# Optimization experiments

Measured on AMD Instinct MI355X. Metric: run time of the kernel, lower is better.

The kernel has to match this reference:

```python
import jax, jax.numpy as jnp
import numpy as np

N, D = 20000, 16          # nodes, fixed in-degree
IN, HID, OUT = 128, 128, 1


def _lstm_final_h(x_seq, Wih, Whh, bih, bhh):
    # x_seq: [D, N, F]; LSTM with hidden size H == F, zero init state.
    # Returns final hidden state h_D: [N, H]. PyTorch gate order i,f,g,o.
    Nn = x_seq.shape[1]
    H = Whh.shape[1]
    b = bih + bhh

    def step(carry, xt):
        h, c = carry
        gates = xt @ Wih.T + h @ Whh.T + b          # [N, 4H]
        i, f, g, o = jnp.split(gates, 4, axis=-1)
        c = jax.nn.sigmoid(f) * c + jax.nn.sigmoid(i) * jnp.tanh(g)
        h = jax.nn.sigmoid(o) * jnp.tanh(c)
        return (h, c), None

    init = (jnp.zeros((Nn, H), x_seq.dtype), jnp.zeros((Nn, H), x_seq.dtype))
    (h, _), _ = jax.lax.scan(step, init, x_seq)
    return h


def _sage_lstm(x, nbr_idx, Wih, Whh, bih, bhh, Wself, Wneigh, bneigh):
    # DGL SAGEConv(aggregator='lstm'): out = fc_self(x) + fc_neigh(lstm(neighbors))
    msgs = x[nbr_idx]                                # gather: [N, D, F]
    hN = _lstm_final_h(jnp.swapaxes(msgs, 0, 1), Wih, Whh, bih, bhh)  # [N, F]
    return x @ Wself.T + hN @ Wneigh.T + bneigh


def setup_inputs() -> dict:
    key = jax.random.key(0)
    ks = jax.random.split(key, 16)
    s = 1.0 / float(np.sqrt(IN))
    u = lambda k, sh: jax.random.uniform(k, sh, jnp.float32, -s, s)
    return {
        "x": jax.random.normal(ks[0], (N, IN), jnp.float32),
        "nbr_idx": jax.random.randint(ks[1], (N, D), 0, N),
        "Wih1": u(ks[2], (4 * IN, IN)), "Whh1": u(ks[3], (4 * IN, IN)),
        "bih1": u(ks[4], (4 * IN,)), "bhh1": u(ks[5], (4 * IN,)),
        "Wself1": u(ks[6], (HID, IN)), "Wneigh1": u(ks[7], (HID, IN)),
        "bneigh1": jnp.zeros((HID,), jnp.float32),
        "Wih2": u(ks[8], (4 * HID, HID)), "Whh2": u(ks[9], (4 * HID, HID)),
        "bih2": u(ks[10], (4 * HID,)), "bhh2": u(ks[11], (4 * HID,)),
        "Wself2": u(ks[12], (OUT, HID)), "Wneigh2": u(ks[13], (OUT, HID)),
        "bneigh2": jnp.zeros((OUT,), jnp.float32),
    }


def reference(x, nbr_idx, Wih1, Whh1, bih1, bhh1, Wself1, Wneigh1, bneigh1,
              Wih2, Whh2, bih2, bhh2, Wself2, Wneigh2, bneigh2):
    h = _sage_lstm(x, nbr_idx, Wih1, Whh1, bih1, bhh1, Wself1, Wneigh1, bneigh1)
    h = jax.nn.relu(h)
    h = _sage_lstm(h, nbr_idx, Wih2, Whh2, bih2, bhh2, Wself2, Wneigh2, bneigh2)
    return jax.nn.sigmoid(h)
```

## Files before the change

### kernel.cpp

```cpp
#include <hip/hip_runtime.h>


#define NN   20000
#define L2E  1.4426950408889634f

typedef unsigned short u16;
typedef __attribute__((ext_vector_type(8))) short frag8;
typedef __attribute__((ext_vector_type(4))) float facc4;
typedef __attribute__((ext_vector_type(8))) _Float16 half8;

#define OFF_X16   0u
#define OFF_H1    5120000u
#define OFF_WIH1P 15360000u
#define OFF_WHH1P 15491072u
#define OFF_WIH2P 15622144u
#define OFF_WHH2P 15753216u
#define OFF_WS1P  15884288u
#define OFF_WN1P  15917056u
#define OFF_WS2B  15949824u
#define OFF_WN2B  15950080u
#define OFF_B1    15950336u
#define OFF_B2    15952384u
#define OFF_XPREA 15954432u
#define OFF_XPREB 36434432u

__device__ __forceinline__ u16 f2bf(float f) {
  union { float f; unsigned u; } v; v.f = f;
  unsigned r = (v.u + 0x7fffu + ((v.u >> 16) & 1u)) >> 16;
  return (u16)r;
}
__device__ __forceinline__ float bflo(unsigned u) {
  union { unsigned u; float f; } v; v.u = u << 16; return v.f;
}
__device__ __forceinline__ float bfhi(unsigned u) {
  union { unsigned u; float f; } v; v.u = u & 0xffff0000u; return v.f;
}
__device__ __forceinline__ unsigned pk2h(float a, float b) {
  union { _Float16 h[2]; unsigned u; } v;
  v.h[0] = (_Float16)a; v.h[1] = (_Float16)b;
  return v.u;
}
__device__ __forceinline__ unsigned pkbf(float a, float b) {
  unsigned r;
  asm("v_cvt_pk_bf16_f32 %0, %1, %2" : "=v"(r) : "v"(a), "v"(b));
  return r;
}
__device__ __forceinline__ facc4 mfma16(frag8 a, frag8 b, facc4 c) {
  return __builtin_amdgcn_mfma_f32_16x16x32_bf16(a, b, c, 0, 0, 0);
}
__device__ __forceinline__ float rcpf(float x) { return __builtin_amdgcn_rcpf(x); }
__device__ __forceinline__ float ex2(float x)  { return __builtin_amdgcn_exp2f(x); }
__device__ __forceinline__ float sigm_ps(float xp) { return rcpf(1.f + ex2(-xp)); }
__device__ __forceinline__ float gate_scale(int row) {
  return (row >= 256 && row < 384) ? 2.f * L2E : L2E;
}
__device__ __forceinline__ float dot2(unsigned a, unsigned b) {
  return bflo(a) * bflo(b) + bfhi(a) * bfhi(b);
}

__device__ __forceinline__ void pack512v(frag8* dst, const float* src, int f) {
  int ln = f & 63, kb = (f >> 6) & 3, tj = f >> 8;
  int row = tj * 16 + (ln & 15);
  int col = kb * 32 + (ln >> 4) * 8;
  float s = gate_scale(row);
  const float* p = src + row * 128 + col;
  float4 v0 = *(const float4*)p;
  float4 v1 = *(const float4*)(p + 4);
  uint4 u = { pkbf(v0.x * s, v0.y * s), pkbf(v0.z * s, v0.w * s),
              pkbf(v1.x * s, v1.y * s), pkbf(v1.z * s, v1.w * s) };
  *(uint4*)&dst[f] = u;
}
__device__ __forceinline__ void pack128v(frag8* dst, const float* src, int f) {
  int ln = f & 63, kb = (f >> 6) & 3, tj = f >> 8;
  const float* p = src + (tj * 16 + (ln & 15)) * 128 + kb * 32 + (ln >> 4) * 8;
  float4 v0 = *(const float4*)p;
  float4 v1 = *(const float4*)(p + 4);
  uint4 u = { pkbf(v0.x, v0.y), pkbf(v0.z, v0.w),
              pkbf(v1.x, v1.y), pkbf(v1.z, v1.w) };
  *(uint4*)&dst[f] = u;
}

__global__ __launch_bounds__(256) void pack_kernel(
    const float* __restrict__ Wih1, const float* __restrict__ Whh1,
    const float* __restrict__ bih1, const float* __restrict__ bhh1,
    const float* __restrict__ Wself1, const float* __restrict__ Wneigh1,
    const float* __restrict__ Wih2, const float* __restrict__ Whh2,
    const float* __restrict__ bih2, const float* __restrict__ bhh2,
    const float* __restrict__ Wself2, const float* __restrict__ Wneigh2,
    char* __restrict__ ws)
{
  int i = blockIdx.x * 256 + threadIdx.x;
  if (i < 8192) { pack512v((frag8*)(ws + OFF_WIH1P), Wih1, i); return; }
  i -= 8192;
  if (i < 8192) { pack512v((frag8*)(ws + OFF_WHH1P), Whh1, i); return; }
  i -= 8192;
  if (i < 8192) { pack512v((frag8*)(ws + OFF_WIH2P), Wih2, i); return; }
  i -= 8192;
  if (i < 8192) { pack512v((frag8*)(ws + OFF_WHH2P), Whh2, i); return; }
  i -= 8192;
  if (i < 2048) { pack128v((frag8*)(ws + OFF_WS1P), Wself1, i); return; }
  i -= 2048;
  if (i < 2048) { pack128v((frag8*)(ws + OFF_WN1P), Wneigh1, i); return; }
  i -= 2048;
  if (i < 128) { ((u16*)(ws + OFF_WS2B))[i] = f2bf(Wself2[i]); return; }
  i -= 128;
  if (i < 128) { ((u16*)(ws + OFF_WN2B))[i] = f2bf(Wneigh2[i]); return; }
  i -= 128;
  if (i < 512) { ((float*)(ws + OFF_B1))[i] = (bih1[i] + bhh1[i]) * gate_scale(i); return; }
  i -= 512;
  if (i < 512) { ((float*)(ws + OFF_B2))[i] = (bih2[i] + bhh2[i]) * gate_scale(i); }
}

__global__ __launch_bounds__(512) void prep1_kernel(
    const float* __restrict__ x,
    const frag8* __restrict__ Wp,
    const float* __restrict__ bias,
    u16* __restrict__ x16,
    u16* __restrict__ xpre)
{
  __shared__ __align__(16) u16 xt[32 * 136];
  __shared__ __align__(16) u16 stage[32 * 520];
  const int tid = threadIdx.x;
  const int base = blockIdx.x * 32;
  {
    int r = tid >> 4, o = (tid & 15) * 8;
    const float* src = x + (size_t)(base + r) * 128 + o;
    float4 v0 = *(const float4*)(src);
    float4 v1 = *(const float4*)(src + 4);
    uint4 st = { pkbf(v0.x, v0.y), pkbf(v0.z, v0.w),
                 pkbf(v1.x, v1.y), pkbf(v1.z, v1.w) };
    *(uint4*)(xt + r * 136 + o) = st;
    *(uint4*)(x16 + (size_t)(base + r) * 128 + o) = st;
  }
  __syncthreads();
  const int lane = tid & 63, wave = tid >> 6;
  const int m = lane & 15, quad = lane >> 4;
  const int rg = wave & 1, jh = wave >> 1;
  const int r = rg * 16 + m;
  frag8 bfr[4];
#pragma unroll
  for (int kb = 0; kb < 4; ++kb)
    bfr[kb] = *(const frag8*)(xt + r * 136 + kb * 32 + quad * 8);
  u16* srow = stage + r * 520;
#pragma unroll
  for (int j = 0; j < 8; ++j) {
    const int tj = jh * 8 + j;
    float4 bv = *(const float4*)(bias + tj * 16 + quad * 4);
    facc4 acc = {bv.x, bv.y, bv.z, bv.w};
#pragma unroll
    for (int kb = 0; kb < 4; ++kb)
      acc = mfma16(Wp[(tj * 4 + kb) * 64 + lane], bfr[kb], acc);
    uint2 st = { pk2h(acc[0], acc[1]), pk2h(acc[2], acc[3]) };
    *(uint2*)(srow + (tj & 7) * 64 + quad * 16 + (tj >> 3) * 4) = st;
  }
  __syncthreads();
#pragma unroll
  for (int i = tid; i < 2048; i += 512) {
    int rr = i >> 6, cc = i & 63;
    ((uint4*)(xpre + (size_t)(base + rr) * 512))[cc] =
        ((const uint4*)(stage + rr * 520))[cc];
  }
}

__device__ __forceinline__ void lstm_core(
    const u16* __restrict__ Xpre, const frag8* __restrict__ Wp,
    const int* __restrict__ nbr, int node_base,
    u16 (*h_lds)[16 * 136], int (*idx_lds)[16])
{
  const int tid = threadIdx.x;
  const int lane = tid & 63, g = tid >> 6;
  const int m = lane & 15, quad = lane >> 4;

  frag8 A[4][4];
#pragma unroll
  for (int gate = 0; gate < 4; ++gate)
#pragma unroll
    for (int kb = 0; kb < 4; ++kb)
      A[gate][kb] = Wp[((gate * 8 + g) * 4 + kb) * 64 + lane];

  for (int i = tid; i < 16 * 136; i += 512) h_lds[0][i] = 0;

  int4 idx4 = *(const int4*)(nbr + (size_t)(node_base + m) * 16 + quad * 4);
  if (g == 0) {
    idx_lds[quad * 4 + 0][m] = idx4.x;
    idx_lds[quad * 4 + 1][m] = idx4.y;
    idx_lds[quad * 4 + 2][m] = idx4.z;
    idx_lds[quad * 4 + 3][m] = idx4.w;
  }

  facc4 c = {0.f, 0.f, 0.f, 0.f};

  int idx0 = __shfl(idx4.x, m, 64);
  const uint4* p0 = (const uint4*)(Xpre + (size_t)idx0 * 512) + g * 8 + quad * 2;
  uint4 pX0 = p0[0], pX1 = p0[1];

  __syncthreads();

#pragma unroll 1
  for (int t = 0; t < 16; ++t) {
    const u16* hr = h_lds[t & 1];
    u16* hw = h_lds[(t + 1) & 1];
    int idxn = idx_lds[t < 15 ? t + 1 : 15][m];
    const uint4* pn = (const uint4*)(Xpre + (size_t)idxn * 512) + g * 8 + quad * 2;

    frag8 bfr[4];
#pragma unroll
    for (int kb = 0; kb < 4; ++kb)
      bfr[kb] = *(const frag8*)(hr + m * 136 + kb * 32 + quad * 8);

    union { uint4 u; half8 h; } ua, ub;
    ua.u = pX0; ub.u = pX1;
    facc4 ai = {(float)ua.h[0], (float)ua.h[1], (float)ua.h[2], (float)ua.h[3]};
    facc4 af = {(float)ua.h[4], (float)ua.h[5], (float)ua.h[6], (float)ua.h[7]};
    facc4 ag = {(float)ub.h[0], (float)ub.h[1], (float)ub.h[2], (float)ub.h[3]};
    facc4 ao = {(float)ub.h[4], (float)ub.h[5], (float)ub.h[6], (float)ub.h[7]};
    pX0 = pn[0]; pX1 = pn[1];

#pragma unroll
    for (int kb = 0; kb < 4; ++kb) {
      ai = mfma16(A[0][kb], bfr[kb], ai);
      af = mfma16(A[1][kb], bfr[kb], af);
      ag = mfma16(A[2][kb], bfr[kb], ag);
      ao = mfma16(A[3][kb], bfr[kb], ao);
    }

    facc4 hv;
#pragma unroll
    for (int r = 0; r < 4; ++r) {
      float ea = ex2(-ai[r]);
      float eg = ex2(fminf(ag[r], 80.f));
      float sitg = (eg - 1.f) * rcpf((1.f + ea) * (1.f + eg));
      float sf = sigm_ps(af[r]);
      float cn = sf * c[r] + sitg;
      c[r] = cn;
      float eo = ex2(-ao[r]);
      float C  = ex2((2.f * L2E) * cn);
      hv[r] = (C - 1.f) * rcpf((1.f + eo) * (1.f + C));
    }
    uint2 hp = { pkbf(hv[0], hv[1]), pkbf(hv[2], hv[3]) };
    *(uint2*)(hw + m * 136 + g * 16 + quad * 4) = hp;
    asm volatile("s_waitcnt lgkmcnt(0)" ::: "memory");
    __builtin_amdgcn_s_barrier();
  }
}

__global__ __launch_bounds__(512, 4) void lstm1_kernel(
    const u16* __restrict__ Xpre, const frag8* __restrict__ Wp,
    const int* __restrict__ nbr, const u16* __restrict__ xin,
    const frag8* __restrict__ Wsp, const frag8* __restrict__ Wnp,
    const float* __restrict__ bias_o,
    const frag8* __restrict__ WihX, const float* __restrict__ biasX,
    u16* __restrict__ xpreOut, u16* __restrict__ h1)
{
  __shared__ __align__(16) u16 h_lds[2][16 * 136];
  __shared__ int idx_lds[16][16];
  __shared__ __align__(16) u16 xstage[16 * 520];
  const int tid = threadIdx.x;
  const int lane = tid & 63, g = tid >> 6;
  const int m = lane & 15, quad = lane >> 4;
  const int node_base = blockIdx.x * 16;

  lstm_core(Xpre, Wp, nbr, node_base, h_lds, idx_lds);
  const u16* hf = h_lds[0];

  const int row = node_base + m;
  frag8 bx[4], bh[4];
#pragma unroll
  for (int kb = 0; kb < 4; ++kb) {
    bx[kb] = *(const frag8*)(xin + (size_t)row * 128 + kb * 32 + quad * 8);
    bh[kb] = *(const frag8*)(hf + m * 136 + kb * 32 + quad * 8);
  }
  float4 bv = *(const float4*)(bias_o + g * 16 + quad * 4);
  facc4 acc = {bv.x, bv.y, bv.z, bv.w};
#pragma unroll
  for (int kb = 0; kb < 4; ++kb) {
    acc = mfma16(Wsp[(g * 4 + kb) * 64 + lane], bx[kb], acc);
    acc = mfma16(Wnp[(g * 4 + kb) * 64 + lane], bh[kb], acc);
  }
  uint2 st = { pkbf(fmaxf(acc[0], 0.f), fmaxf(acc[1], 0.f)),
               pkbf(fmaxf(acc[2], 0.f), fmaxf(acc[3], 0.f)) };
  u16* stg = (u16*)h_lds[1];
  *(uint2*)(stg + m * 136 + g * 16 + quad * 4) = st;
  __syncthreads();
  {
    const int r = tid >> 5, cc = tid & 31;
    *(uint2*)(h1 + (size_t)(node_base + r) * 128 + cc * 4) =
        *(const uint2*)(stg + r * 136 + cc * 4);
  }
  frag8 b2f[4];
#pragma unroll
  for (int kb = 0; kb < 4; ++kb)
    b2f[kb] = *(const frag8*)(stg + m * 136 + kb * 32 + quad * 8);
#pragma unroll
  for (int j = 0; j < 4; ++j) {
    const int tj = g * 4 + j;
    float4 bx2 = *(const float4*)(biasX + tj * 16 + quad * 4);
    facc4 acc2 = {bx2.x, bx2.y, bx2.z, bx2.w};
#pragma unroll
    for (int kb = 0; kb < 4; ++kb)
      acc2 = mfma16(WihX[(tj * 4 + kb) * 64 + lane], b2f[kb], acc2);
    uint2 st2 = { pk2h(acc2[0], acc2[1]), pk2h(acc2[2], acc2[3]) };
    *(uint2*)(xstage + m * 520 + (tj & 7) * 64 + quad * 16 + (tj >> 3) * 4) = st2;
  }
  __syncthreads();
#pragma unroll
  for (int i = tid; i < 1024; i += 512) {
    int rr = i >> 6, cc = i & 63;
    ((uint4*)(xpreOut + (size_t)(node_base + rr) * 512))[cc] =
        ((const uint4*)(xstage + rr * 520))[cc];
  }
}

__global__ __launch_bounds__(512, 4) void lstm2_kernel(
    const u16* __restrict__ Xpre, const frag8* __restrict__ Wp,
    const int* __restrict__ nbr,
    const u16* __restrict__ ws2, const u16* __restrict__ wn2,
    const float* __restrict__ b2o,
    const u16* __restrict__ h1, float* __restrict__ outp)
{
  __shared__ __align__(16) u16 h_lds[2][16 * 136];
  __shared__ int idx_lds[16][16];
  const int tid = threadIdx.x;
  const int node_base = blockIdx.x * 16;

  lstm_core(Xpre, Wp, nbr, node_base, h_lds, idx_lds);
  const u16* hf = h_lds[0];

  const int n = tid >> 5, cc = tid & 31;
  uint2 a = *(const uint2*)(h1 + (size_t)(node_base + n) * 128 + cc * 4);
  uint2 w = *(const uint2*)(ws2 + cc * 4);
  uint2 b = *(const uint2*)(hf + n * 136 + cc * 4);
  uint2 v = *(const uint2*)(wn2 + cc * 4);
  float p = dot2(a.x, w.x) + dot2(a.y, w.y) + dot2(b.x, v.x) + dot2(b.y, v.y);
#pragma unroll
  for (int s = 1; s < 32; s <<= 1) p += __shfl_xor(p, s, 64);
  if (cc == 0) {
    float acc = p + b2o[0];
    outp[node_base + n] = rcpf(1.f + ex2(-acc * L2E));
  }
}

extern "C" void kernel_launch(void* const* d_in, const int* in_sizes, int n_in,
                              void* d_out, int out_size, void* d_ws, size_t ws_size,
                              hipStream_t stream) {
  const float* x       = (const float*)d_in[0];
  const int*   nbr     = (const int*)d_in[1];
  const float* Wih1    = (const float*)d_in[2];
  const float* Whh1    = (const float*)d_in[3];
  const float* bih1    = (const float*)d_in[4];
  const float* bhh1    = (const float*)d_in[5];
  const float* Wself1  = (const float*)d_in[6];
  const float* Wneigh1 = (const float*)d_in[7];
  const float* bneigh1 = (const float*)d_in[8];
  const float* Wih2    = (const float*)d_in[9];
  const float* Whh2    = (const float*)d_in[10];
  const float* bih2    = (const float*)d_in[11];
  const float* bhh2    = (const float*)d_in[12];
  const float* Wself2  = (const float*)d_in[13];
  const float* Wneigh2 = (const float*)d_in[14];
  const float* bneigh2 = (const float*)d_in[15];

  char* ws = (char*)d_ws;
  u16*   x16   = (u16*)(ws + OFF_X16);
  u16*   h1    = (u16*)(ws + OFF_H1);
  u16*   XpreA = (u16*)(ws + OFF_XPREA);
  u16*   XpreB = (u16*)(ws + OFF_XPREB);
  frag8* Wih1p = (frag8*)(ws + OFF_WIH1P);
  frag8* Whh1p = (frag8*)(ws + OFF_WHH1P);
  frag8* Wih2p = (frag8*)(ws + OFF_WIH2P);
  frag8* Whh2p = (frag8*)(ws + OFF_WHH2P);
  frag8* Ws1p  = (frag8*)(ws + OFF_WS1P);
  frag8* Wn1p  = (frag8*)(ws + OFF_WN1P);
  u16*   Ws2b  = (u16*)(ws + OFF_WS2B);
  u16*   Wn2b  = (u16*)(ws + OFF_WN2B);
  float* b1    = (float*)(ws + OFF_B1);
  float* b2    = (float*)(ws + OFF_B2);

  pack_kernel<<<149, 256, 0, stream>>>(Wih1, Whh1, bih1, bhh1, Wself1,
                                       Wneigh1, Wih2, Whh2, bih2, bhh2,
                                       Wself2, Wneigh2, ws);
  prep1_kernel<<<625, 512, 0, stream>>>(x, Wih1p, b1, x16, XpreA);
  lstm1_kernel<<<1250, 512, 0, stream>>>(XpreA, Whh1p, nbr, x16, Ws1p, Wn1p,
                                         bneigh1, Wih2p, b2, XpreB, h1);
  lstm2_kernel<<<1250, 512, 0, stream>>>(XpreB, Whh2p, nbr, Ws2b, Wn2b,
                                         bneigh2, h1, (float*)d_out);
}
```

Baseline: 238.5 us.

## Precompute layer-2 self term in lstm1 and stagger odd blocks with sleep

The layer-2 self projection (h1 · Wself2) is now computed in lstm1's epilogue and stored as one float per node. lstm2 then reads that scalar instead of re-reading the full bf16 h1 row, which cuts its global traffic. A short s_sleep is also added for odd blocks before the recurrent loop, to desynchronise the gather bursts of co-resident blocks. The sleep adds a fixed delay to half of the blocks and may only help if memory contention is the limit.

```diff
diff --git a/kernel.cpp b/kernel.cpp
--- a/kernel.cpp
+++ b/kernel.cpp
@@ -11,6 +11,7 @@
 
 #define OFF_X16   0u
 #define OFF_H1    5120000u
+#define OFF_S1    10240000u
 #define OFF_WIH1P 15360000u
 #define OFF_WHH1P 15491072u
 #define OFF_WIH2P 15622144u
@@ -194,6 +195,8 @@
   const uint4* p0 = (const uint4*)(Xpre + (size_t)idx0 * 512) + g * 8 + quad * 2;
   uint4 pX0 = p0[0], pX1 = p0[1];
 
+  if (blockIdx.x & 1) __builtin_amdgcn_s_sleep(32);
+
   __syncthreads();
 
 #pragma unroll 1
@@ -250,7 +253,8 @@
     const frag8* __restrict__ Wsp, const frag8* __restrict__ Wnp,
     const float* __restrict__ bias_o,
     const frag8* __restrict__ WihX, const float* __restrict__ biasX,
-    u16* __restrict__ xpreOut, u16* __restrict__ h1)
+    const u16* __restrict__ ws2,
+    u16* __restrict__ xpreOut, u16* __restrict__ h1, float* __restrict__ s1)
 {
   __shared__ __align__(16) u16 h_lds[2][16 * 136];
   __shared__ int idx_lds[16][16];
@@ -284,8 +288,13 @@
   __syncthreads();
   {
     const int r = tid >> 5, cc = tid & 31;
-    *(uint2*)(h1 + (size_t)(node_base + r) * 128 + cc * 4) =
-        *(const uint2*)(stg + r * 136 + cc * 4);
+    uint2 hv2 = *(const uint2*)(stg + r * 136 + cc * 4);
+    *(uint2*)(h1 + (size_t)(node_base + r) * 128 + cc * 4) = hv2;
+    uint2 w = *(const uint2*)(ws2 + cc * 4);
+    float p = dot2(hv2.x, w.x) + dot2(hv2.y, w.y);
+#pragma unroll
+    for (int s = 1; s < 32; s <<= 1) p += __shfl_xor(p, s, 64);
+    if (cc == 0) s1[node_base + r] = p;
   }
   frag8 b2f[4];
 #pragma unroll
@@ -314,9 +323,8 @@
 __global__ __launch_bounds__(512, 4) void lstm2_kernel(
     const u16* __restrict__ Xpre, const frag8* __restrict__ Wp,
     const int* __restrict__ nbr,
-    const u16* __restrict__ ws2, const u16* __restrict__ wn2,
-    const float* __restrict__ b2o,
-    const u16* __restrict__ h1, float* __restrict__ outp)
+    const u16* __restrict__ wn2, const float* __restrict__ b2o,
+    const float* __restrict__ s1, float* __restrict__ outp)
 {
   __shared__ __align__(16) u16 h_lds[2][16 * 136];
   __shared__ int idx_lds[16][16];
@@ -327,15 +335,14 @@
   const u16* hf = h_lds[0];
 
   const int n = tid >> 5, cc = tid & 31;
-  uint2 a = *(const uint2*)(h1 + (size_t)(node_base + n) * 128 + cc * 4);
-  uint2 w = *(const uint2*)(ws2 + cc * 4);
+  float s1n = s1[node_base + n];
   uint2 b = *(const uint2*)(hf + n * 136 + cc * 4);
   uint2 v = *(const uint2*)(wn2 + cc * 4);
-  float p = dot2(a.x, w.x) + dot2(a.y, w.y) + dot2(b.x, v.x) + dot2(b.y, v.y);
+  float p = dot2(b.x, v.x) + dot2(b.y, v.y);
 #pragma unroll
   for (int s = 1; s < 32; s <<= 1) p += __shfl_xor(p, s, 64);
   if (cc == 0) {
-    float acc = p + b2o[0];
+    float acc = p + s1n + b2o[0];
     outp[node_base + n] = rcpf(1.f + ex2(-acc * L2E));
   }
 }
@@ -363,6 +370,7 @@
   char* ws = (char*)d_ws;
   u16*   x16   = (u16*)(ws + OFF_X16);
   u16*   h1    = (u16*)(ws + OFF_H1);
+  float* s1    = (float*)(ws + OFF_S1);
   u16*   XpreA = (u16*)(ws + OFF_XPREA);
   u16*   XpreB = (u16*)(ws + OFF_XPREB);
   frag8* Wih1p = (frag8*)(ws + OFF_WIH1P);
@@ -381,7 +389,8 @@
                                        Wself2, Wneigh2, ws);
   prep1_kernel<<<625, 512, 0, stream>>>(x, Wih1p, b1, x16, XpreA);
   lstm1_kernel<<<1250, 512, 0, stream>>>(XpreA, Whh1p, nbr, x16, Ws1p, Wn1p,
-                                         bneigh1, Wih2p, b2, XpreB, h1);
-  lstm2_kernel<<<1250, 512, 0, stream>>>(XpreB, Whh2p, nbr, Ws2b, Wn2b,
-                                         bneigh2, h1, (float*)d_out);
-}
+                                         bneigh1, Wih2p, b2, Ws2b,
+                                         XpreB, h1, s1);
+  lstm2_kernel<<<1250, 512, 0, stream>>>(XpreB, Whh2p, nbr, Wn2b, bneigh2,
+                                         s1, (float*)d_out);
+}
```

Measured after the change: 238.8 us. No clear change (+0.1%).
